# Kernel optimization log

Hardware: AMD Instinct MI355X
Metric: run time of the kernel (lower is better)

The kernel has to match this reference:

```python
import math
import jax, jax.numpy as jnp
import numpy as np

DIM = 2048
HEAD_DIM = 64
N_HEADS = DIM // HEAD_DIM
BATCH = 4
SEQ = 1025  # 32*32 axial positions + 1 zero position
EPS = 1e-6


def make_theta(head_dim=HEAD_DIM, h=32, w=32):
    # freqs: geometric from pi to 10*pi, head_dim//4 of them
    n_freqs = head_dim // 4
    freqs = jnp.exp(jnp.linspace(math.log(math.pi), math.log(10 * math.pi), n_freqs))
    hp = jnp.linspace(-1.0, 1.0, h + 1)
    wp = jnp.linspace(-1.0, 1.0, w + 1)
    hp = (hp[:-1] + hp[1:]) / 2
    wp = (wp[:-1] + wp[1:]) / 2
    pos = jnp.stack(jnp.meshgrid(hp, wp, indexing='ij'), axis=-1).reshape(h * w, 2)
    pos = jnp.concatenate([jnp.zeros((1, 2)), pos], axis=0)  # [1025, 2]
    theta_h = pos[:, 0:1] * freqs  # [S, n_freqs]
    theta_w = pos[:, 1:2] * freqs
    return jnp.concatenate([theta_h, theta_w], axis=-1)  # [S, head_dim//2]


def rms_norm(x, scale, eps=EPS):
    mean_sq = jnp.mean(jnp.square(x.astype(jnp.float32)), axis=-1, keepdims=True)
    s = scale.astype(jnp.float32) * jax.lax.rsqrt(mean_sq + eps)
    return (x * s.astype(x.dtype)).astype(x.dtype)


def apply_rotary(x, theta):
    # x: [B, H, S, D], theta: [S, d] with 2*d <= D
    d = theta.shape[-1]
    x1, x2, x3 = x[..., :d], x[..., d:2 * d], x[..., 2 * d:]
    cos, sin = jnp.cos(theta), jnp.sin(theta)  # broadcast over B, H
    y1 = x1 * cos - x2 * sin
    y2 = x2 * cos + x1 * sin
    return jnp.concatenate([y1, y2, x3], axis=-1)


def setup_inputs() -> dict:
    key = jax.random.key(0)
    k1, k2, k3 = jax.random.split(key, 3)
    x = jax.random.normal(k1, (BATCH, SEQ, DIM), dtype=jnp.float32)
    scale = jnp.ones((DIM,), dtype=jnp.float32)
    w_qkv = jax.random.normal(k2, (3 * DIM, DIM), dtype=jnp.float32) * 0.02
    w_out = jax.random.normal(k3, (DIM, DIM), dtype=jnp.float32) * 0.02
    return {"x": x, "scale": scale, "w_qkv": w_qkv, "w_out": w_out}


def reference(x, scale, w_qkv, w_out):
    B, S, _ = x.shape
    skip = x
    h = rms_norm(x, scale)
    qkv = h @ w_qkv.T  # [B, S, 3*DIM]
    qkv = qkv.reshape(B, S, 3, N_HEADS, HEAD_DIM)
    qkv = jnp.transpose(qkv, (0, 3, 2, 1, 4))  # [B, H, 3, S, D]
    q, k, v = qkv[:, :, 0], qkv[:, :, 1], qkv[:, :, 2]
    theta = make_theta()[:S]
    q = apply_rotary(q, theta)
    k = apply_rotary(k, theta)
    scores = jnp.einsum('bhqd,bhkd->bhqk', q, k) / math.sqrt(HEAD_DIM)
    causal = jnp.tril(jnp.ones((S, S), dtype=bool))
    scores = jnp.where(causal, scores, jnp.finfo(scores.dtype).min)
    attn = jax.nn.softmax(scores, axis=-1)
    o = jnp.einsum('bhqk,bhkd->bhqd', attn, v)  # [B, H, S, D]
    o = jnp.transpose(o, (0, 2, 1, 3)).reshape(B, S, DIM)
    return o @ w_out.T + skip
```

## Files before the change

kernel.cpp:

```cpp
#include <hip/hip_runtime.h>
#include <hip/hip_bf16.h>
#include <cstdint>

#define SEQ   1025
#define SPAD  1088
#define DIM   2048
#define NQKV  6144
#define MROWS 4100
#define MPAD  4352
#define NH    32

typedef __attribute__((ext_vector_type(8))) short bf16x8;
typedef __attribute__((ext_vector_type(4))) short bf16x4;
typedef __attribute__((ext_vector_type(4))) float f32x4;

#define MFMA16x16(A,B,C) __builtin_amdgcn_mfma_f32_16x16x32_bf16(A,B,C,0,0,0)

static __device__ __forceinline__ float bf2f(short s) {
    union { unsigned int u; float f; } v;
    v.u = ((unsigned int)(unsigned short)s) << 16;
    return v.f;
}
static __device__ __forceinline__ short f2bf(float f) {
    union { float f; unsigned int u; } v; v.f = f;
    unsigned int r = v.u + 0x7fffu + ((v.u >> 16) & 1u);
    return (short)(r >> 16);
}

typedef __attribute__((address_space(1))) unsigned int u32g;
typedef __attribute__((address_space(3))) unsigned int u32l;
static __device__ __forceinline__ void gld_lds16(void* lds, const void* g) {
    __builtin_amdgcn_global_load_lds((const u32g*)(uintptr_t)g,
                                     (u32l*)(uintptr_t)lds, 16, 0, 0);
}

#define SBX() __builtin_amdgcn_sched_barrier(0)
#define PRIO(x) __builtin_amdgcn_s_setprio(x)
#define VMCNT(n) asm volatile("s_waitcnt vmcnt(" #n ")" ::: "memory")
#define LGKM(n)  asm volatile("s_waitcnt lgkmcnt(" #n ")" ::: "memory")

__global__ __launch_bounds__(256) void trig_k(float* __restrict__ cosT, float* __restrict__ sinT) {
    int i = blockIdx.x * 256 + threadIdx.x;
    if (i >= SEQ * 16) return;
    int s = i >> 4, f = i & 15;
    float ph = 0.f, pw = 0.f;
    if (s > 0) {
        int p = s - 1;
        ph = -1.f + ((p >> 5) + 0.5f) * 0.0625f;
        pw = -1.f + ((p & 31) + 0.5f) * 0.0625f;
    }
    double fr = 3.141592653589793 * exp((double)f * 0.15350567286626973);
    float th = (float)(ph * fr), tw = (float)(pw * fr);
    cosT[s*32 + f]      = cosf(th);
    sinT[s*32 + f]      = sinf(th);
    cosT[s*32 + 16 + f] = cosf(tw);
    sinT[s*32 + 16 + f] = sinf(tw);
}

__global__ __launch_bounds__(256) void rmsnorm_k(const float* __restrict__ x,
                                                 const float* __restrict__ sc,
                                                 short* __restrict__ h) {
    int row = blockIdx.x, t = threadIdx.x;
    short* hr = h + (size_t)row * DIM;
    if (row >= MROWS) {
        bf16x8 z = {};
        *(bf16x8*)(hr + t*8) = z;
        return;
    }
    const float4* xr = (const float4*)(x + (size_t)row * DIM);
    float4 a = xr[2*t], b = xr[2*t+1];
    float ss = a.x*a.x + a.y*a.y + a.z*a.z + a.w*a.w
             + b.x*b.x + b.y*b.y + b.z*b.z + b.w*b.w;
    #pragma unroll
    for (int off = 32; off; off >>= 1) ss += __shfl_xor(ss, off, 64);
    __shared__ float red[4];
    if ((t & 63) == 0) red[t >> 6] = ss;
    __syncthreads();
    float ms = (red[0]+red[1]+red[2]+red[3]) * (1.0f/2048.0f);
    float inv = rsqrtf(ms + 1e-6f);
    const float4* sr = (const float4*)sc;
    float4 s0 = sr[2*t], s1 = sr[2*t+1];
    bf16x8 o;
    o[0]=f2bf(a.x*(s0.x*inv)); o[1]=f2bf(a.y*(s0.y*inv));
    o[2]=f2bf(a.z*(s0.z*inv)); o[3]=f2bf(a.w*(s0.w*inv));
    o[4]=f2bf(b.x*(s1.x*inv)); o[5]=f2bf(b.y*(s1.y*inv));
    o[6]=f2bf(b.z*(s1.z*inv)); o[7]=f2bf(b.w*(s1.w*inv));
    *(bf16x8*)(hr + t*8) = o;
}

__global__ __launch_bounds__(256) void conv2_k(const float* __restrict__ a, short* __restrict__ oa, int n4a,
                                               const float* __restrict__ b, short* __restrict__ ob, int n4b) {
    int i = blockIdx.x * 256 + threadIdx.x;
    const float* src; short* dst; int j;
    if (i < n4a) { src = a; dst = oa; j = i; }
    else { j = i - n4a; if (j >= n4b) return; src = b; dst = ob; }
    float4 v = ((const float4*)src)[j];
    bf16x4 r = { f2bf(v.x), f2bf(v.y), f2bf(v.z), f2bf(v.w) };
    *(bf16x4*)(dst + (size_t)j*4) = r;
}

template<int EPI>
__global__ __launch_bounds__(512, 2) void gemm8p(const short* __restrict__ A,
                                                 const short* __restrict__ B,
                                                 void* __restrict__ C,
                                                 const float* __restrict__ skip,
                                                 int N, int K, int nbm) {
    extern __shared__ char smem[];
    const int nwg = gridDim.x;
    const int cpx = nwg >> 3;
    const int bid = blockIdx.x;
    const int sid = (bid & 7) * cpx + (bid >> 3);
    const int bm = sid % nbm;
    const int bn = sid / nbm;

    const int t = threadIdx.x, w = t >> 6, l = t & 63;
    const int lr = l & 15, lg = l >> 4;
    const int wr = w >> 2, wc = w & 3;

    const short* Ab = A + (size_t)bm * 256 * K;
    const short* Bb = B + (size_t)bn * 256 * K;

    const int srow = t >> 3;
    const int scol = (((t & 7) ^ (srow & 7)) << 3);

    const int cs0 = (lg * 16) ^ ((lr & 7) << 4);
    const int cs1 = (64 + lg * 16) ^ ((lr & 7) << 4);
    const int aBase = wr * 16384 + lr * 128;
    const int bBase = 32768 + (wc >> 1) * 16384 + ((wc & 1) * 64 + lr) * 128;

    f32x4 acc[8][4] = {};
    bf16x8 rA[4][2], rB01[2][2], rB23[2][2];

#define STAGE_A(kt, half, bb) do {                                            \
    const int k0_ = (kt) * 64;                                                \
    gld_lds16(smem + (bb)*65536 + (half)*16384 + (w<<10),                     \
              Ab + (size_t)((half)*128 + srow) * K + k0_ + scol);             \
    gld_lds16(smem + (bb)*65536 + (half)*16384 + 8192 + (w<<10),              \
              Ab + (size_t)((half)*128 + 64 + srow) * K + k0_ + scol);        \
} while (0)

#define STAGE_B(kt, half, bb) do {                                            \
    const int k0_ = (kt) * 64;                                                \
    gld_lds16(smem + (bb)*65536 + 32768 + (half)*16384 + (w<<10),             \
              Bb + (size_t)((half)*128 + srow) * K + k0_ + scol);             \
    gld_lds16(smem + (bb)*65536 + 32768 + (half)*16384 + 8192 + (w<<10),      \
              Bb + (size_t)((half)*128 + 64 + srow) * K + k0_ + scol);        \
} while (0)

#define READ_A(bb, h) do {                                                    \
    const char* p_ = smem + (bb)*65536 + aBase + (h)*8192;                    \
    _Pragma("unroll")                                                         \
    for (int am = 0; am < 4; ++am) {                                          \
        rA[am][0] = *(const bf16x8*)(p_ + am*2048 + cs0);                     \
        rA[am][1] = *(const bf16x8*)(p_ + am*2048 + cs1);                     \
    }                                                                         \
} while (0)

#define READ_B(bb, np, arr) do {                                              \
    const char* p_ = smem + (bb)*65536 + bBase + (np)*4096;                   \
    _Pragma("unroll")                                                         \
    for (int nn = 0; nn < 2; ++nn) {                                          \
        arr[nn][0] = *(const bf16x8*)(p_ + nn*2048 + cs0);                    \
        arr[nn][1] = *(const bf16x8*)(p_ + nn*2048 + cs1);                    \
    }                                                                         \
} while (0)

#define MF_Q(h, np, arr) do {                                                 \
    _Pragma("unroll")                                                         \
    for (int am = 0; am < 4; ++am)                                            \
    _Pragma("unroll")                                                         \
    for (int nn = 0; nn < 2; ++nn) {                                          \
        acc[(h)*4+am][(np)*2+nn] =                                            \
            MFMA16x16(rA[am][0], arr[nn][0], acc[(h)*4+am][(np)*2+nn]);       \
        acc[(h)*4+am][(np)*2+nn] =                                            \
            MFMA16x16(rA[am][1], arr[nn][1], acc[(h)*4+am][(np)*2+nn]);       \
    }                                                                         \
} while (0)

#define BOPEN()  do { SBX(); __builtin_amdgcn_s_barrier(); LGKM(0); SBX(); } while (0)
#define BOPEN_NL() do { SBX(); __builtin_amdgcn_s_barrier(); SBX(); } while (0)
#define BCLOSE() do { SBX(); __builtin_amdgcn_s_barrier(); SBX(); } while (0)

    STAGE_B(0, 0, 0); STAGE_B(0, 1, 0);
    STAGE_A(0, 0, 0); STAGE_A(0, 1, 0);
    STAGE_B(1, 0, 1); STAGE_B(1, 1, 1);
    VMCNT(4); SBX();
    __builtin_amdgcn_s_barrier(); SBX();

    const int NT2 = K / 128;
    for (int it = 0; it < NT2; ++it) {
        const bool more = (it < NT2 - 1);
        READ_A(0, 0); READ_B(0, 0, rB01);
        STAGE_A(2*it + 1, 0, 1);
        LGKM(8);
        BOPEN(); PRIO(1); MF_Q(0, 0, rB01); PRIO(0); BCLOSE();
        READ_B(0, 1, rB23);
        STAGE_A(2*it + 1, 1, 1);
        BOPEN(); PRIO(1); MF_Q(0, 1, rB23); PRIO(0); BCLOSE();
        READ_A(0, 1);
        if (more) STAGE_B(2*it + 2, 0, 0);
        BOPEN(); PRIO(1); MF_Q(1, 1, rB23); PRIO(0); BCLOSE();
        if (more) STAGE_B(2*it + 2, 1, 0);
        BOPEN_NL(); PRIO(1); MF_Q(1, 0, rB01); PRIO(0); SBX();
        if (more) { VMCNT(4); } else { VMCNT(0); }
        BCLOSE();
        READ_A(1, 0); READ_B(1, 0, rB01);
        if (more) STAGE_A(2*it + 2, 0, 0);
        LGKM(8);
        BOPEN(); PRIO(1); MF_Q(0, 0, rB01); PRIO(0); BCLOSE();
        READ_B(1, 1, rB23);
        if (more) STAGE_A(2*it + 2, 1, 0);
        BOPEN(); PRIO(1); MF_Q(0, 1, rB23); PRIO(0); BCLOSE();
        READ_A(1, 1);
        if (more) STAGE_B(2*it + 3, 0, 1);
        BOPEN(); PRIO(1); MF_Q(1, 1, rB23); PRIO(0); BCLOSE();
        if (more) STAGE_B(2*it + 3, 1, 1);
        BOPEN_NL(); PRIO(1); MF_Q(1, 0, rB01); PRIO(0); SBX();
        if (more) { VMCNT(4); }
        BCLOSE();
    }

    #pragma unroll
    for (int m = 0; m < 8; ++m) {
        const int row0 = bm*256 + wr*128 + m*16 + lg*4;
        #pragma unroll
        for (int n = 0; n < 4; ++n) {
            const int col = bn*256 + wc*64 + n*16 + lr;
            #pragma unroll
            for (int r = 0; r < 4; ++r) {
                const int row = row0 + r;
                if constexpr (EPI == 0) {
                    ((short*)C)[(size_t)row * N + col] = f2bf(acc[m][n][r]);
                } else {
                    if (row < MROWS)
                        ((float*)C)[(size_t)row * N + col] =
                            acc[m][n][r] + skip[(size_t)row * N + col];
                }
            }
        }
    }
#undef STAGE_A
#undef STAGE_B
#undef READ_A
#undef READ_B
#undef MF_Q
#undef BOPEN
#undef BOPEN_NL
#undef BCLOSE
}

__global__ __launch_bounds__(256) void rearrange_k(const short* __restrict__ qkv,
        const float* __restrict__ cosT, const float* __restrict__ sinT,
        short* __restrict__ kr, short* __restrict__ vt) {
    int bid = blockIdx.x;
    int bh = bid / 17, st = bid % 17;
    int b = bh >> 5, hh = bh & 31;
    int s0 = st * 64;
    int t = threadIdx.x;
    __shared__ short vs[64][68];
    #pragma unroll
    for (int i = 0; i < 8; ++i) {
        int task = t + i*256;
        int sl = task >> 5, p = task & 31;
        int s = s0 + sl;
        float y1 = 0.f, y2 = 0.f;
        if (s < SEQ) {
            const short* src = qkv + (size_t)(b*SEQ + s)*NQKV + DIM + hh*64;
            float x1 = bf2f(src[p]), x2 = bf2f(src[32+p]);
            float c = cosT[s*32+p], sn = sinT[s*32+p];
            y1 = x1*c - x2*sn;
            y2 = x2*c + x1*sn;
        }
        short* dst = kr + ((size_t)bh*SPAD + s)*64;
        dst[p]    = f2bf(y1);
        dst[32+p] = f2bf(y2);
    }
    #pragma unroll
    for (int i = 0; i < 16; ++i) {
        int task = t + i*256;
        int sl = task >> 6, d = task & 63;
        int s = s0 + sl;
        short v = 0;
        if (s < SEQ) v = qkv[(size_t)(b*SEQ + s)*NQKV + 2*DIM + hh*64 + d];
        vs[sl][d] = v;
    }
    __syncthreads();
    #pragma unroll
    for (int i = 0; i < 16; ++i) {
        int task = t + i*256;
        int d = task >> 6, sl = task & 63;
        vt[((size_t)bh*64 + d)*SPAD + s0 + sl] = vs[sl][d];
    }
}

__global__ __launch_bounds__(256) void attn_k(const short* __restrict__ qkv,
        const short* __restrict__ kr, const short* __restrict__ vt,
        const float* __restrict__ cosT, const float* __restrict__ sinT,
        short* __restrict__ ob) {
    const int nwg = gridDim.x;
    const int cpx = nwg >> 3;
    const int bid = blockIdx.x;
    const int sid = (bid & 7) * cpx + (bid >> 3);
    const int bh = sid / 17;
    const int qt = sid % 17;
    const int q0 = qt * 64;
    const int b = bh >> 5, hh = bh & 31;
    const int t = threadIdx.x, w = t >> 6, l = t & 63;
    const int lr = l & 15, lg = l >> 4;

    __shared__ short Ks[2][64*64];
    __shared__ short Vts[2][64*64];

    const int qrow = q0 + w*16 + lr;
    const int qc = qrow < SEQ ? qrow : SEQ-1;
    const short* qsrc = qkv + (size_t)(b*SEQ + qc)*NQKV + hh*64;
    bf16x8 xlo = *(const bf16x8*)(qsrc + lg*8);
    bf16x8 xhi = *(const bf16x8*)(qsrc + 32 + lg*8);
    const float4* cp = (const float4*)(cosT + qc*32 + lg*8);
    const float4* sp = (const float4*)(sinT + qc*32 + lg*8);
    float cc[8], sn[8];
    { float4 u = cp[0], v2 = cp[1];
      cc[0]=u.x; cc[1]=u.y; cc[2]=u.z; cc[3]=u.w;
      cc[4]=v2.x; cc[5]=v2.y; cc[6]=v2.z; cc[7]=v2.w; }
    { float4 u = sp[0], v2 = sp[1];
      sn[0]=u.x; sn[1]=u.y; sn[2]=u.z; sn[3]=u.w;
      sn[4]=v2.x; sn[5]=v2.y; sn[6]=v2.z; sn[7]=v2.w; }
    bf16x8 qf0, qf1;
    #pragma unroll
    for (int j = 0; j < 8; ++j) {
        float x1 = bf2f(xlo[j]), x2 = bf2f(xhi[j]);
        qf0[j] = f2bf(x1*cc[j] - x2*sn[j]);
        qf1[j] = f2bf(x2*cc[j] + x1*sn[j]);
    }

    f32x4 oacc[4] = {};
    float mrun = -1e30f, lrun = 0.f;
    const int ntile = qt + 1;
    const float SC = 0.125f * 1.4426950408889634f;

    const char* kbase = (const char*)(kr + (size_t)bh * SPAD * 64);
    const char* vbase = (const char*)(vt + (size_t)bh * 64 * SPAD);
    const int srow8 = l >> 3;
    const int sslotB = ((l & 7) ^ srow8) << 4;
    const int swz = (lr & 7) << 4;

#define STAGE_KV(kt, c) do {                                                   \
    const int kv0_ = (kt) * 64;                                                \
    gld_lds16((char*)Ks[c] + w*2048,                                           \
              kbase + (size_t)(kv0_ + w*16 + srow8)*128 + sslotB);             \
    gld_lds16((char*)Ks[c] + w*2048 + 1024,                                    \
              kbase + (size_t)(kv0_ + w*16 + 8 + srow8)*128 + sslotB);         \
    gld_lds16((char*)Vts[c] + w*2048,                                          \
              vbase + (size_t)(w*16 + srow8)*(SPAD*2) + (size_t)kv0_*2 + sslotB); \
    gld_lds16((char*)Vts[c] + w*2048 + 1024,                                   \
              vbase + (size_t)(w*16 + 8 + srow8)*(SPAD*2) + (size_t)kv0_*2 + sslotB); \
} while (0)

    STAGE_KV(0, 0);

    for (int kt = 0; kt < ntile; ++kt) {
        const int kv0 = kt * 64;
        const int cur = kt & 1;
        if (kt + 1 < ntile) { STAGE_KV(kt + 1, cur ^ 1); SBX(); VMCNT(4); }
        else { SBX(); VMCNT(0); }
        SBX(); __builtin_amdgcn_s_barrier(); SBX();

        f32x4 st[4];
        #pragma unroll
        for (int f = 0; f < 4; ++f) {
            const char* kp = (const char*)Ks[cur] + (f*16 + lr)*128;
            bf16x8 a0 = *(const bf16x8*)(kp + ((lg*16) ^ swz));
            bf16x8 a1 = *(const bf16x8*)(kp + ((64 + lg*16) ^ swz));
            f32x4 z = {};
            z = MFMA16x16(a0, qf0, z);
            st[f] = MFMA16x16(a1, qf1, z);
        }

        float pv[16];
        float tmax = -1e30f;
        #pragma unroll
        for (int f = 0; f < 4; ++f)
        #pragma unroll
        for (int r = 0; r < 4; ++r) {
            int kv = kv0 + f*16 + lg*4 + r;
            float v = st[f][r] * SC;
            v = (kv <= qrow && kv < SEQ) ? v : -1e30f;
            pv[f*4+r] = v; tmax = fmaxf(tmax, v);
        }
        tmax = fmaxf(tmax, __shfl_xor(tmax, 16, 64));
        tmax = fmaxf(tmax, __shfl_xor(tmax, 32, 64));
        float mnew = fmaxf(mrun, tmax);
        float alpha = exp2f(mrun - mnew);
        float psum = 0.f;
        bf16x8 pf0, pf1;
        #pragma unroll
        for (int j = 0; j < 4; ++j) {
            float p0 = exp2f(pv[0*4+j] - mnew);
            float p1 = exp2f(pv[1*4+j] - mnew);
            float p2 = exp2f(pv[2*4+j] - mnew);
            float p3 = exp2f(pv[3*4+j] - mnew);
            psum += (p0 + p1) + (p2 + p3);
            pf0[j] = f2bf(p0); pf0[4+j] = f2bf(p1);
            pf1[j] = f2bf(p2); pf1[4+j] = f2bf(p3);
        }
        psum += __shfl_xor(psum, 16, 64);
        psum += __shfl_xor(psum, 32, 64);
        lrun = lrun * alpha + psum;
        mrun = mnew;
        #pragma unroll
        for (int df = 0; df < 4; ++df) {
            oacc[df][0] *= alpha; oacc[df][1] *= alpha;
            oacc[df][2] *= alpha; oacc[df][3] *= alpha;
        }
        #pragma unroll
        for (int df = 0; df < 4; ++df) {
            const char* vp = (const char*)Vts[cur] + (df*16 + lr)*128;
            bf16x4 v0 = *(const bf16x4*)(vp + ((lg*8) ^ swz));
            bf16x4 v1 = *(const bf16x4*)(vp + ((32 + lg*8) ^ swz));
            bf16x4 v2 = *(const bf16x4*)(vp + ((64 + lg*8) ^ swz));
            bf16x4 v3 = *(const bf16x4*)(vp + ((96 + lg*8) ^ swz));
            bf16x8 vf0, vf1;
            vf0[0]=v0[0]; vf0[1]=v0[1]; vf0[2]=v0[2]; vf0[3]=v0[3];
            vf0[4]=v1[0]; vf0[5]=v1[1]; vf0[6]=v1[2]; vf0[7]=v1[3];
            vf1[0]=v2[0]; vf1[1]=v2[1]; vf1[2]=v2[2]; vf1[3]=v2[3];
            vf1[4]=v3[0]; vf1[5]=v3[1]; vf1[6]=v3[2]; vf1[7]=v3[3];
            oacc[df] = MFMA16x16(vf0, pf0, oacc[df]);
            oacc[df] = MFMA16x16(vf1, pf1, oacc[df]);
        }
        SBX(); __builtin_amdgcn_s_barrier(); SBX();
    }
#undef STAGE_KV

    if (qrow < SEQ) {
        float inv = 1.0f / lrun;
        short* orow = ob + (size_t)(b*SEQ + qrow)*DIM + hh*64;
        #pragma unroll
        for (int df = 0; df < 4; ++df) {
            bf16x4 ov = { f2bf(oacc[df][0]*inv), f2bf(oacc[df][1]*inv),
                          f2bf(oacc[df][2]*inv), f2bf(oacc[df][3]*inv) };
            *(bf16x4*)(orow + df*16 + lg*4) = ov;
        }
    }
}

extern "C" void kernel_launch(void* const* d_in, const int* in_sizes, int n_in,
                              void* d_out, int out_size, void* d_ws, size_t ws_size,
                              hipStream_t stream) {
    const float* x     = (const float*)d_in[0];
    const float* scale = (const float*)d_in[1];
    const float* w_qkv = (const float*)d_in[2];
    const float* w_out = (const float*)d_in[3];
    float* out = (float*)d_out;

    char* ws = (char*)d_ws;
    size_t off = 0;
    auto alloc = [&](size_t bytes) -> char* {
        char* p = ws + off;
        off += (bytes + 255) & ~(size_t)255;
        return p;
    };
    float* cosT  = (float*)alloc((size_t)SEQ*32*4);
    float* sinT  = (float*)alloc((size_t)SEQ*32*4);
    short* h_b   = (short*)alloc((size_t)MPAD*DIM*2);
    short* wq_b  = (short*)alloc((size_t)NQKV*DIM*2);
    short* wo_b  = (short*)alloc((size_t)DIM*DIM*2);
    short* qkv_b = (short*)alloc((size_t)MPAD*NQKV*2);
    short* k_r   = (short*)alloc((size_t)128*SPAD*64*2);
    short* vt    = (short*)alloc((size_t)128*SPAD*64*2);
    short* o_b   = h_b;

    hipFuncSetAttribute((const void*)gemm8p<0>,
                        hipFuncAttributeMaxDynamicSharedMemorySize, 131072);
    hipFuncSetAttribute((const void*)gemm8p<1>,
                        hipFuncAttributeMaxDynamicSharedMemorySize, 131072);

    trig_k<<<65, 256, 0, stream>>>(cosT, sinT);
    rmsnorm_k<<<MPAD, 256, 0, stream>>>(x, scale, h_b);
    conv2_k<<<(NQKV*DIM/4 + DIM*DIM/4 + 255)/256, 256, 0, stream>>>(
        w_qkv, wq_b, NQKV*DIM/4, w_out, wo_b, DIM*DIM/4);
    gemm8p<0><<<(MPAD/256)*(NQKV/256), 512, 131072, stream>>>(h_b, wq_b, qkv_b, nullptr, NQKV, DIM, MPAD/256);
    rearrange_k<<<128*17, 256, 0, stream>>>(qkv_b, cosT, sinT, k_r, vt);
    attn_k<<<17*128, 256, 0, stream>>>(qkv_b, k_r, vt, cosT, sinT, o_b);
    gemm8p<1><<<(MPAD/256)*(DIM/256), 512, 131072, stream>>>(o_b, wo_b, out, x, DIM, DIM, MPAD/256);
}
```

Baseline: 440.1 us.

## Load K/V fragments directly from global into registers, dropping LDS staging

The attention kernel no longer stages K and V^T tiles through double-buffered shared memory with barriers. Each wave now loads its MFMA fragments straight from global memory into registers, software-pipelining the K fragments across two register sets and loading V fragments at the start of each tile. This removes LDS traffic and the two block barriers per tile, but each of the four waves now fetches the full K/V tile itself (4x global/L2 traffic) and register pressure grows.

Result: slower. 621.9 us (+41.3%).

```diff
diff --git a/kernel.cpp b/kernel.cpp
--- a/kernel.cpp
+++ b/kernel.cpp
@@ -308,9 +308,6 @@
     const int t = threadIdx.x, w = t >> 6, l = t & 63;
     const int lr = l & 15, lg = l >> 4;
 
-    __shared__ short Ks[2][64*64];
-    __shared__ short Vts[2][64*64];
-
     const int qrow = q0 + w*16 + lr;
     const int qc = qrow < SEQ ? qrow : SEQ-1;
     const short* qsrc = qkv + (size_t)(b*SEQ + qc)*NQKV + hh*64;
@@ -338,98 +335,96 @@
     const int ntile = qt + 1;
     const float SC = 0.125f * 1.4426950408889634f;
 
-    const char* kbase = (const char*)(kr + (size_t)bh * SPAD * 64);
-    const char* vbase = (const char*)(vt + (size_t)bh * 64 * SPAD);
-    const int srow8 = l >> 3;
-    const int sslotB = ((l & 7) ^ srow8) << 4;
-    const int swz = (lr & 7) << 4;
-
-#define STAGE_KV(kt, c) do {                                                   \
-    const int kv0_ = (kt) * 64;                                                \
-    gld_lds16((char*)Ks[c] + w*2048,                                           \
-              kbase + (size_t)(kv0_ + w*16 + srow8)*128 + sslotB);             \
-    gld_lds16((char*)Ks[c] + w*2048 + 1024,                                    \
-              kbase + (size_t)(kv0_ + w*16 + 8 + srow8)*128 + sslotB);         \
-    gld_lds16((char*)Vts[c] + w*2048,                                          \
-              vbase + (size_t)(w*16 + srow8)*(SPAD*2) + (size_t)kv0_*2 + sslotB); \
-    gld_lds16((char*)Vts[c] + w*2048 + 1024,                                   \
-              vbase + (size_t)(w*16 + 8 + srow8)*(SPAD*2) + (size_t)kv0_*2 + sslotB); \
-} while (0)
-
-    STAGE_KV(0, 0);
-
-    for (int kt = 0; kt < ntile; ++kt) {
-        const int kv0 = kt * 64;
-        const int cur = kt & 1;
-        if (kt + 1 < ntile) { STAGE_KV(kt + 1, cur ^ 1); SBX(); VMCNT(4); }
-        else { SBX(); VMCNT(0); }
-        SBX(); __builtin_amdgcn_s_barrier(); SBX();
-
-        f32x4 st[4];
-        #pragma unroll
-        for (int f = 0; f < 4; ++f) {
-            const char* kp = (const char*)Ks[cur] + (f*16 + lr)*128;
-            bf16x8 a0 = *(const bf16x8*)(kp + ((lg*16) ^ swz));
-            bf16x8 a1 = *(const bf16x8*)(kp + ((64 + lg*16) ^ swz));
-            f32x4 z = {};
-            z = MFMA16x16(a0, qf0, z);
-            st[f] = MFMA16x16(a1, qf1, z);
-        }
-
-        float pv[16];
-        float tmax = -1e30f;
-        #pragma unroll
-        for (int f = 0; f < 4; ++f)
-        #pragma unroll
-        for (int r = 0; r < 4; ++r) {
-            int kv = kv0 + f*16 + lg*4 + r;
-            float v = st[f][r] * SC;
-            v = (kv <= qrow && kv < SEQ) ? v : -1e30f;
-            pv[f*4+r] = v; tmax = fmaxf(tmax, v);
-        }
-        tmax = fmaxf(tmax, __shfl_xor(tmax, 16, 64));
-        tmax = fmaxf(tmax, __shfl_xor(tmax, 32, 64));
-        float mnew = fmaxf(mrun, tmax);
-        float alpha = exp2f(mrun - mnew);
-        float psum = 0.f;
-        bf16x8 pf0, pf1;
-        #pragma unroll
-        for (int j = 0; j < 4; ++j) {
-            float p0 = exp2f(pv[0*4+j] - mnew);
-            float p1 = exp2f(pv[1*4+j] - mnew);
-            float p2 = exp2f(pv[2*4+j] - mnew);
-            float p3 = exp2f(pv[3*4+j] - mnew);
-            psum += (p0 + p1) + (p2 + p3);
-            pf0[j] = f2bf(p0); pf0[4+j] = f2bf(p1);
-            pf1[j] = f2bf(p2); pf1[4+j] = f2bf(p3);
-        }
-        psum += __shfl_xor(psum, 16, 64);
-        psum += __shfl_xor(psum, 32, 64);
-        lrun = lrun * alpha + psum;
-        mrun = mnew;
-        #pragma unroll
-        for (int df = 0; df < 4; ++df) {
-            oacc[df][0] *= alpha; oacc[df][1] *= alpha;
-            oacc[df][2] *= alpha; oacc[df][3] *= alpha;
-        }
-        #pragma unroll
-        for (int df = 0; df < 4; ++df) {
-            const char* vp = (const char*)Vts[cur] + (df*16 + lr)*128;
-            bf16x4 v0 = *(const bf16x4*)(vp + ((lg*8) ^ swz));
-            bf16x4 v1 = *(const bf16x4*)(vp + ((32 + lg*8) ^ swz));
-            bf16x4 v2 = *(const bf16x4*)(vp + ((64 + lg*8) ^ swz));
-            bf16x4 v3 = *(const bf16x4*)(vp + ((96 + lg*8) ^ swz));
-            bf16x8 vf0, vf1;
-            vf0[0]=v0[0]; vf0[1]=v0[1]; vf0[2]=v0[2]; vf0[3]=v0[3];
-            vf0[4]=v1[0]; vf0[5]=v1[1]; vf0[6]=v1[2]; vf0[7]=v1[3];
-            vf1[0]=v2[0]; vf1[1]=v2[1]; vf1[2]=v2[2]; vf1[3]=v2[3];
-            vf1[4]=v3[0]; vf1[5]=v3[1]; vf1[6]=v3[2]; vf1[7]=v3[3];
-            oacc[df] = MFMA16x16(vf0, pf0, oacc[df]);
-            oacc[df] = MFMA16x16(vf1, pf1, oacc[df]);
-        }
-        SBX(); __builtin_amdgcn_s_barrier(); SBX();
-    }
-#undef STAGE_KV
+    const char* kfp = (const char*)(kr + (size_t)bh * SPAD * 64) + (size_t)lr*128 + lg*16;
+    const char* vfp = (const char*)(vt + (size_t)bh * 64 * SPAD) + (size_t)lr*2176 + lg*8;
+
+#define LOADK(dst, kt_) do {                                                   \
+    const char* kp_ = kfp + (size_t)(kt_) * 8192;                              \
+    _Pragma("unroll")                                                          \
+    for (int f = 0; f < 4; ++f) {                                              \
+        dst[f*2]   = *(const bf16x8*)(kp_ + f*2048);                           \
+        dst[f*2+1] = *(const bf16x8*)(kp_ + f*2048 + 64);                      \
+    }                                                                          \
+} while (0)
+
+#define BODY(ka, kt_) do {                                                     \
+    const int kv0 = (kt_) * 64;                                                \
+                             \
+    bf16x4 vv[16];                                                             \
+    { const char* vp_ = vfp + (size_t)kv0 * 2;                                 \
+      _Pragma("unroll")                                                        \
+      for (int df = 0; df < 4; ++df)                                           \
+      _Pragma("unroll")                                                        \
+      for (int s2 = 0; s2 < 4; ++s2)                                           \
+          vv[df*4+s2] = *(const bf16x4*)(vp_ + (size_t)df*16*2176 + s2*32); }  \
+    f32x4 st[4];                                                               \
+    _Pragma("unroll")                                                          \
+    for (int f = 0; f < 4; ++f) {                                              \
+        f32x4 z = {};                                                          \
+        z = MFMA16x16(ka[f*2], qf0, z);                                        \
+        st[f] = MFMA16x16(ka[f*2+1], qf1, z);                                  \
+    }                                                                          \
+    float tmax = -1e30f;                                                       \
+    _Pragma("unroll")                                                          \
+    for (int f = 0; f < 4; ++f)                                                \
+    _Pragma("unroll")                                                          \
+    for (int r = 0; r < 4; ++r) {                                              \
+        int kv = kv0 + f*16 + lg*4 + r;                                        \
+        float v = st[f][r] * SC;                                               \
+        v = (kv <= qrow && kv < SEQ) ? v : -1e30f;                             \
+        st[f][r] = v; tmax = fmaxf(tmax, v);                                   \
+    }                                                                          \
+    tmax = fmaxf(tmax, __shfl_xor(tmax, 16, 64));                              \
+    tmax = fmaxf(tmax, __shfl_xor(tmax, 32, 64));                              \
+    float mnew = fmaxf(mrun, tmax);                                            \
+    float alpha = exp2f(mrun - mnew);                                          \
+    float psum = 0.f;                                                          \
+    bf16x8 pf0, pf1;                                                           \
+    _Pragma("unroll")                                                          \
+    for (int j = 0; j < 4; ++j) {                                              \
+        float p0 = exp2f(st[0][j] - mnew);                                     \
+        float p1 = exp2f(st[1][j] - mnew);                                     \
+        float p2 = exp2f(st[2][j] - mnew);                                     \
+        float p3 = exp2f(st[3][j] - mnew);                                     \
+        psum += (p0 + p1) + (p2 + p3);                                         \
+        pf0[j] = f2bf(p0); pf0[4+j] = f2bf(p1);                                \
+        pf1[j] = f2bf(p2); pf1[4+j] = f2bf(p3);                                \
+    }                                                                          \
+    psum += __shfl_xor(psum, 16, 64);                                          \
+    psum += __shfl_xor(psum, 32, 64);                                          \
+    lrun = lrun * alpha + psum;                                                \
+    mrun = mnew;                                                               \
+    _Pragma("unroll")                                                          \
+    for (int df = 0; df < 4; ++df) {                                           \
+        oacc[df][0] *= alpha; oacc[df][1] *= alpha;                            \
+        oacc[df][2] *= alpha; oacc[df][3] *= alpha;                            \
+    }                                                                          \
+    _Pragma("unroll")                                                          \
+    for (int df = 0; df < 4; ++df) {                                           \
+        bf16x8 vf0, vf1;                                                       \
+        bf16x4 a_ = vv[df*4+0], b_ = vv[df*4+1], c_ = vv[df*4+2], d_ = vv[df*4+3]; \
+        vf0[0]=a_[0]; vf0[1]=a_[1]; vf0[2]=a_[2]; vf0[3]=a_[3];                \
+        vf0[4]=b_[0]; vf0[5]=b_[1]; vf0[6]=b_[2]; vf0[7]=b_[3];                \
+        vf1[0]=c_[0]; vf1[1]=c_[1]; vf1[2]=c_[2]; vf1[3]=c_[3];                \
+        vf1[4]=d_[0]; vf1[5]=d_[1]; vf1[6]=d_[2]; vf1[7]=d_[3];                \
+        oacc[df] = MFMA16x16(vf0, pf0, oacc[df]);                              \
+        oacc[df] = MFMA16x16(vf1, pf1, oacc[df]);                              \
+    }                                                                          \
+} while (0)
+
+    bf16x8 kA[8], kB[8];
+    LOADK(kA, 0);
+    int kt = 0;
+    for (;;) {
+        if (kt + 1 < ntile) LOADK(kB, kt + 1);
+        BODY(kA, kt);
+        ++kt; if (kt >= ntile) break;
+        if (kt + 1 < ntile) LOADK(kA, kt + 1);
+        BODY(kB, kt);
+        ++kt; if (kt >= ntile) break;
+    }
+#undef LOADK
+#undef BODY
 
     if (qrow < SEQ) {
         float inv = 1.0f / lrun;
```

## Double attention query tile per workgroup and fuse prologue kernels into one launch

Applied to the files above, without the earlier changes.

Attention workgroups now process 128 query rows, with each wave computing two 16-row groups against the same staged K/V tiles. This halves K/V LDS staging per query, and tiles are scheduled longest-first. The rmsnorm, weight conversion and trig table kernels are merged into a single launch to cut launch overhead. The wider tile raises register pressure and does some extra masked work on the causal diagonal.

After: 450.5 us. 2.3% more time.

```diff
diff --git a/kernel.cpp b/kernel.cpp
--- a/kernel.cpp
+++ b/kernel.cpp
@@ -39,8 +39,57 @@
 #define VMCNT(n) asm volatile("s_waitcnt vmcnt(" #n ")" ::: "memory")
 #define LGKM(n)  asm volatile("s_waitcnt lgkmcnt(" #n ")" ::: "memory")
 
-__global__ __launch_bounds__(256) void trig_k(float* __restrict__ cosT, float* __restrict__ sinT) {
-    int i = blockIdx.x * 256 + threadIdx.x;
+__global__ __launch_bounds__(256) void prep_k(const float* __restrict__ x,
+        const float* __restrict__ sc, short* __restrict__ h,
+        const float* __restrict__ wq, short* __restrict__ wqb,
+        const float* __restrict__ wo, short* __restrict__ wob,
+        float* __restrict__ cosT, float* __restrict__ sinT) {
+    __shared__ float red[4];
+    int blk = blockIdx.x, t = threadIdx.x;
+    if (blk < MPAD) {
+        int row = blk;
+        short* hr = h + (size_t)row * DIM;
+        if (row >= MROWS) {
+            bf16x8 z = {};
+            *(bf16x8*)(hr + t*8) = z;
+            return;
+        }
+        const float4* xr = (const float4*)(x + (size_t)row * DIM);
+        float4 a = xr[2*t], b2 = xr[2*t+1];
+        float ss = a.x*a.x + a.y*a.y + a.z*a.z + a.w*a.w
+                 + b2.x*b2.x + b2.y*b2.y + b2.z*b2.z + b2.w*b2.w;
+        #pragma unroll
+        for (int off = 32; off; off >>= 1) ss += __shfl_xor(ss, off, 64);
+        if ((t & 63) == 0) red[t >> 6] = ss;
+        __syncthreads();
+        float ms = (red[0]+red[1]+red[2]+red[3]) * (1.0f/2048.0f);
+        float inv = rsqrtf(ms + 1e-6f);
+        const float4* sr = (const float4*)sc;
+        float4 s0 = sr[2*t], s1 = sr[2*t+1];
+        bf16x8 o;
+        o[0]=f2bf(a.x*(s0.x*inv));  o[1]=f2bf(a.y*(s0.y*inv));
+        o[2]=f2bf(a.z*(s0.z*inv));  o[3]=f2bf(a.w*(s0.w*inv));
+        o[4]=f2bf(b2.x*(s1.x*inv)); o[5]=f2bf(b2.y*(s1.y*inv));
+        o[6]=f2bf(b2.z*(s1.z*inv)); o[7]=f2bf(b2.w*(s1.w*inv));
+        *(bf16x8*)(hr + t*8) = o;
+        return;
+    }
+    blk -= MPAD;
+    constexpr int N4A = NQKV*DIM/4;
+    constexpr int N4B = DIM*DIM/4;
+    constexpr int NCB = (N4A + N4B + 255)/256;
+    if (blk < NCB) {
+        int i = blk*256 + t;
+        const float* src; short* dst; int j;
+        if (i < N4A) { src = wq; dst = wqb; j = i; }
+        else { j = i - N4A; if (j >= N4B) return; src = wo; dst = wob; }
+        float4 v = ((const float4*)src)[j];
+        bf16x4 r = { f2bf(v.x), f2bf(v.y), f2bf(v.z), f2bf(v.w) };
+        *(bf16x4*)(dst + (size_t)j*4) = r;
+        return;
+    }
+    blk -= NCB;
+    int i = blk*256 + t;
     if (i >= SEQ * 16) return;
     int s = i >> 4, f = i & 15;
     float ph = 0.f, pw = 0.f;
@@ -55,48 +104,6 @@
     sinT[s*32 + f]      = sinf(th);
     cosT[s*32 + 16 + f] = cosf(tw);
     sinT[s*32 + 16 + f] = sinf(tw);
-}
-
-__global__ __launch_bounds__(256) void rmsnorm_k(const float* __restrict__ x,
-                                                 const float* __restrict__ sc,
-                                                 short* __restrict__ h) {
-    int row = blockIdx.x, t = threadIdx.x;
-    short* hr = h + (size_t)row * DIM;
-    if (row >= MROWS) {
-        bf16x8 z = {};
-        *(bf16x8*)(hr + t*8) = z;
-        return;
-    }
-    const float4* xr = (const float4*)(x + (size_t)row * DIM);
-    float4 a = xr[2*t], b = xr[2*t+1];
-    float ss = a.x*a.x + a.y*a.y + a.z*a.z + a.w*a.w
-             + b.x*b.x + b.y*b.y + b.z*b.z + b.w*b.w;
-    #pragma unroll
-    for (int off = 32; off; off >>= 1) ss += __shfl_xor(ss, off, 64);
-    __shared__ float red[4];
-    if ((t & 63) == 0) red[t >> 6] = ss;
-    __syncthreads();
-    float ms = (red[0]+red[1]+red[2]+red[3]) * (1.0f/2048.0f);
-    float inv = rsqrtf(ms + 1e-6f);
-    const float4* sr = (const float4*)sc;
-    float4 s0 = sr[2*t], s1 = sr[2*t+1];
-    bf16x8 o;
-    o[0]=f2bf(a.x*(s0.x*inv)); o[1]=f2bf(a.y*(s0.y*inv));
-    o[2]=f2bf(a.z*(s0.z*inv)); o[3]=f2bf(a.w*(s0.w*inv));
-    o[4]=f2bf(b.x*(s1.x*inv)); o[5]=f2bf(b.y*(s1.y*inv));
-    o[6]=f2bf(b.z*(s1.z*inv)); o[7]=f2bf(b.w*(s1.w*inv));
-    *(bf16x8*)(hr + t*8) = o;
-}
-
-__global__ __launch_bounds__(256) void conv2_k(const float* __restrict__ a, short* __restrict__ oa, int n4a,
-                                               const float* __restrict__ b, short* __restrict__ ob, int n4b) {
-    int i = blockIdx.x * 256 + threadIdx.x;
-    const float* src; short* dst; int j;
-    if (i < n4a) { src = a; dst = oa; j = i; }
-    else { j = i - n4a; if (j >= n4b) return; src = b; dst = ob; }
-    float4 v = ((const float4*)src)[j];
-    bf16x4 r = { f2bf(v.x), f2bf(v.y), f2bf(v.z), f2bf(v.w) };
-    *(bf16x4*)(dst + (size_t)j*4) = r;
 }
 
 template<int EPI>
@@ -301,9 +308,9 @@
     const int cpx = nwg >> 3;
     const int bid = blockIdx.x;
     const int sid = (bid & 7) * cpx + (bid >> 3);
-    const int bh = sid / 17;
-    const int qt = sid % 17;
-    const int q0 = qt * 64;
+    const int bh = sid / 9;
+    const int qt = 8 - (sid % 9);
+    const int q0 = qt * 128;
     const int b = bh >> 5, hh = bh & 31;
     const int t = threadIdx.x, w = t >> 6, l = t & 63;
     const int lr = l & 15, lg = l >> 4;
@@ -311,31 +318,35 @@
     __shared__ short Ks[2][64*64];
     __shared__ short Vts[2][64*64];
 
-    const int qrow = q0 + w*16 + lr;
-    const int qc = qrow < SEQ ? qrow : SEQ-1;
-    const short* qsrc = qkv + (size_t)(b*SEQ + qc)*NQKV + hh*64;
-    bf16x8 xlo = *(const bf16x8*)(qsrc + lg*8);
-    bf16x8 xhi = *(const bf16x8*)(qsrc + 32 + lg*8);
-    const float4* cp = (const float4*)(cosT + qc*32 + lg*8);
-    const float4* sp = (const float4*)(sinT + qc*32 + lg*8);
-    float cc[8], sn[8];
-    { float4 u = cp[0], v2 = cp[1];
-      cc[0]=u.x; cc[1]=u.y; cc[2]=u.z; cc[3]=u.w;
-      cc[4]=v2.x; cc[5]=v2.y; cc[6]=v2.z; cc[7]=v2.w; }
-    { float4 u = sp[0], v2 = sp[1];
-      sn[0]=u.x; sn[1]=u.y; sn[2]=u.z; sn[3]=u.w;
-      sn[4]=v2.x; sn[5]=v2.y; sn[6]=v2.z; sn[7]=v2.w; }
-    bf16x8 qf0, qf1;
-    #pragma unroll
-    for (int j = 0; j < 8; ++j) {
-        float x1 = bf2f(xlo[j]), x2 = bf2f(xhi[j]);
-        qf0[j] = f2bf(x1*cc[j] - x2*sn[j]);
-        qf1[j] = f2bf(x2*cc[j] + x1*sn[j]);
-    }
-
-    f32x4 oacc[4] = {};
-    float mrun = -1e30f, lrun = 0.f;
-    const int ntile = qt + 1;
+    const int qrowA = q0 + w*32 + lr;
+    const int qrowB = qrowA + 16;
+
+    bf16x8 qf0A, qf1A, qf0B, qf1B;
+    auto loadq = [&](int qrow, bf16x8& f0, bf16x8& f1) {
+        int qc = qrow < SEQ ? qrow : SEQ-1;
+        const short* qsrc = qkv + (size_t)(b*SEQ + qc)*NQKV + hh*64;
+        bf16x8 xlo = *(const bf16x8*)(qsrc + lg*8);
+        bf16x8 xhi = *(const bf16x8*)(qsrc + 32 + lg*8);
+        float4 c0 = ((const float4*)(cosT + qc*32 + lg*8))[0];
+        float4 c1 = ((const float4*)(cosT + qc*32 + lg*8))[1];
+        float4 s0 = ((const float4*)(sinT + qc*32 + lg*8))[0];
+        float4 s1 = ((const float4*)(sinT + qc*32 + lg*8))[1];
+        float cc[8] = {c0.x,c0.y,c0.z,c0.w,c1.x,c1.y,c1.z,c1.w};
+        float sn[8] = {s0.x,s0.y,s0.z,s0.w,s1.x,s1.y,s1.z,s1.w};
+        #pragma unroll
+        for (int j = 0; j < 8; ++j) {
+            float x1 = bf2f(xlo[j]), x2 = bf2f(xhi[j]);
+            f0[j] = f2bf(x1*cc[j] - x2*sn[j]);
+            f1[j] = f2bf(x2*cc[j] + x1*sn[j]);
+        }
+    };
+    loadq(qrowA, qf0A, qf1A);
+    loadq(qrowB, qf0B, qf1B);
+
+    f32x4 oaccA[4] = {}, oaccB[4] = {};
+    float mrunA = -1e30f, lrunA = 0.f;
+    float mrunB = -1e30f, lrunB = 0.f;
+    const int ntile = min(2*qt + 2, 17);
     const float SC = 0.125f * 1.4426950408889634f;
 
     const char* kbase = (const char*)(kr + (size_t)bh * SPAD * 64);
@@ -344,8 +355,8 @@
     const int sslotB = ((l & 7) ^ srow8) << 4;
     const int swz = (lr & 7) << 4;
 
-#define STAGE_KV(kt, c) do {                                                   \
-    const int kv0_ = (kt) * 64;                                                \
+#define STAGE_KV(kt_, c) do {                                                  \
+    const int kv0_ = (kt_) * 64;                                               \
     gld_lds16((char*)Ks[c] + w*2048,                                           \
               kbase + (size_t)(kv0_ + w*16 + srow8)*128 + sslotB);             \
     gld_lds16((char*)Ks[c] + w*2048 + 1024,                                    \
@@ -356,6 +367,38 @@
               vbase + (size_t)(w*16 + 8 + srow8)*(SPAD*2) + (size_t)kv0_*2 + sslotB); \
 } while (0)
 
+#define SOFTMAX(st, qrow, pf0, pf1, mrun, lrun, alpha) do {                    \
+    float tmax = -1e30f;                                                       \
+    _Pragma("unroll")                                                          \
+    for (int f = 0; f < 4; ++f)                                                \
+    _Pragma("unroll")                                                          \
+    for (int r = 0; r < 4; ++r) {                                              \
+        int kv = kv0 + f*16 + lg*4 + r;                                        \
+        float v = st[f][r] * SC;                                               \
+        v = (kv <= (qrow) && kv < SEQ) ? v : -1e30f;                           \
+        st[f][r] = v; tmax = fmaxf(tmax, v);                                   \
+    }                                                                          \
+    tmax = fmaxf(tmax, __shfl_xor(tmax, 16, 64));                              \
+    tmax = fmaxf(tmax, __shfl_xor(tmax, 32, 64));                              \
+    float mnew = fmaxf(mrun, tmax);                                            \
+    alpha = exp2f(mrun - mnew);                                                \
+    float psum = 0.f;                                                          \
+    _Pragma("unroll")                                                          \
+    for (int j = 0; j < 4; ++j) {                                              \
+        float p0 = exp2f(st[0][j] - mnew);                                     \
+        float p1 = exp2f(st[1][j] - mnew);                                     \
+        float p2 = exp2f(st[2][j] - mnew);                                     \
+        float p3 = exp2f(st[3][j] - mnew);                                     \
+        psum += (p0 + p1) + (p2 + p3);                                         \
+        pf0[j] = f2bf(p0); pf0[4+j] = f2bf(p1);                                \
+        pf1[j] = f2bf(p2); pf1[4+j] = f2bf(p3);                                \
+    }                                                                          \
+    psum += __shfl_xor(psum, 16, 64);                                          \
+    psum += __shfl_xor(psum, 32, 64);                                          \
+    lrun = lrun * alpha + psum;                                                \
+    mrun = mnew;                                                               \
+} while (0)
+
     STAGE_KV(0, 0);
 
     for (int kt = 0; kt < ntile; ++kt) {
@@ -365,53 +408,33 @@
         else { SBX(); VMCNT(0); }
         SBX(); __builtin_amdgcn_s_barrier(); SBX();
 
-        f32x4 st[4];
+        f32x4 stA[4], stB[4];
         #pragma unroll
         for (int f = 0; f < 4; ++f) {
             const char* kp = (const char*)Ks[cur] + (f*16 + lr)*128;
             bf16x8 a0 = *(const bf16x8*)(kp + ((lg*16) ^ swz));
             bf16x8 a1 = *(const bf16x8*)(kp + ((64 + lg*16) ^ swz));
-            f32x4 z = {};
-            z = MFMA16x16(a0, qf0, z);
-            st[f] = MFMA16x16(a1, qf1, z);
-        }
-
-        float pv[16];
-        float tmax = -1e30f;
-        #pragma unroll
-        for (int f = 0; f < 4; ++f)
-        #pragma unroll
-        for (int r = 0; r < 4; ++r) {
-            int kv = kv0 + f*16 + lg*4 + r;
-            float v = st[f][r] * SC;
-            v = (kv <= qrow && kv < SEQ) ? v : -1e30f;
-            pv[f*4+r] = v; tmax = fmaxf(tmax, v);
-        }
-        tmax = fmaxf(tmax, __shfl_xor(tmax, 16, 64));
-        tmax = fmaxf(tmax, __shfl_xor(tmax, 32, 64));
-        float mnew = fmaxf(mrun, tmax);
-        float alpha = exp2f(mrun - mnew);
-        float psum = 0.f;
-        bf16x8 pf0, pf1;
-        #pragma unroll
-        for (int j = 0; j < 4; ++j) {
-            float p0 = exp2f(pv[0*4+j] - mnew);
-            float p1 = exp2f(pv[1*4+j] - mnew);
-            float p2 = exp2f(pv[2*4+j] - mnew);
-            float p3 = exp2f(pv[3*4+j] - mnew);
-            psum += (p0 + p1) + (p2 + p3);
-            pf0[j] = f2bf(p0); pf0[4+j] = f2bf(p1);
-            pf1[j] = f2bf(p2); pf1[4+j] = f2bf(p3);
-        }
-        psum += __shfl_xor(psum, 16, 64);
-        psum += __shfl_xor(psum, 32, 64);
-        lrun = lrun * alpha + psum;
-        mrun = mnew;
+            f32x4 zA = {};
+            zA = MFMA16x16(a0, qf0A, zA);
+            stA[f] = MFMA16x16(a1, qf1A, zA);
+            f32x4 zB = {};
+            zB = MFMA16x16(a0, qf0B, zB);
+            stB[f] = MFMA16x16(a1, qf1B, zB);
+        }
+
+        bf16x8 pfA0, pfA1, pfB0, pfB1;
+        float alphaA, alphaB;
+        SOFTMAX(stA, qrowA, pfA0, pfA1, mrunA, lrunA, alphaA);
+        SOFTMAX(stB, qrowB, pfB0, pfB1, mrunB, lrunB, alphaB);
+
         #pragma unroll
         for (int df = 0; df < 4; ++df) {
-            oacc[df][0] *= alpha; oacc[df][1] *= alpha;
-            oacc[df][2] *= alpha; oacc[df][3] *= alpha;
-        }
+            oaccA[df][0] *= alphaA; oaccA[df][1] *= alphaA;
+            oaccA[df][2] *= alphaA; oaccA[df][3] *= alphaA;
+            oaccB[df][0] *= alphaB; oaccB[df][1] *= alphaB;
+            oaccB[df][2] *= alphaB; oaccB[df][3] *= alphaB;
+        }
+
         #pragma unroll
         for (int df = 0; df < 4; ++df) {
             const char* vp = (const char*)Vts[cur] + (df*16 + lr)*128;
@@ -424,23 +447,30 @@
             vf0[4]=v1[0]; vf0[5]=v1[1]; vf0[6]=v1[2]; vf0[7]=v1[3];
             vf1[0]=v2[0]; vf1[1]=v2[1]; vf1[2]=v2[2]; vf1[3]=v2[3];
             vf1[4]=v3[0]; vf1[5]=v3[1]; vf1[6]=v3[2]; vf1[7]=v3[3];
-            oacc[df] = MFMA16x16(vf0, pf0, oacc[df]);
-            oacc[df] = MFMA16x16(vf1, pf1, oacc[df]);
+            oaccA[df] = MFMA16x16(vf0, pfA0, oaccA[df]);
+            oaccA[df] = MFMA16x16(vf1, pfA1, oaccA[df]);
+            oaccB[df] = MFMA16x16(vf0, pfB0, oaccB[df]);
+            oaccB[df] = MFMA16x16(vf1, pfB1, oaccB[df]);
         }
         SBX(); __builtin_amdgcn_s_barrier(); SBX();
     }
 #undef STAGE_KV
-
-    if (qrow < SEQ) {
-        float inv = 1.0f / lrun;
-        short* orow = ob + (size_t)(b*SEQ + qrow)*DIM + hh*64;
-        #pragma unroll
-        for (int df = 0; df < 4; ++df) {
-            bf16x4 ov = { f2bf(oacc[df][0]*inv), f2bf(oacc[df][1]*inv),
-                          f2bf(oacc[df][2]*inv), f2bf(oacc[df][3]*inv) };
-            *(bf16x4*)(orow + df*16 + lg*4) = ov;
-        }
-    }
+#undef SOFTMAX
+
+    auto writeo = [&](int qrow, const f32x4* oacc, float lrun) {
+        if (qrow < SEQ) {
+            float inv = 1.0f / lrun;
+            short* orow = ob + (size_t)(b*SEQ + qrow)*DIM + hh*64;
+            #pragma unroll
+            for (int df = 0; df < 4; ++df) {
+                bf16x4 ov = { f2bf(oacc[df][0]*inv), f2bf(oacc[df][1]*inv),
+                              f2bf(oacc[df][2]*inv), f2bf(oacc[df][3]*inv) };
+                *(bf16x4*)(orow + df*16 + lg*4) = ov;
+            }
+        }
+    };
+    writeo(qrowA, oaccA, lrunA);
+    writeo(qrowB, oaccB, lrunB);
 }
 
 extern "C" void kernel_launch(void* const* d_in, const int* in_sizes, int n_in,
@@ -474,12 +504,11 @@
     hipFuncSetAttribute((const void*)gemm8p<1>,
                         hipFuncAttributeMaxDynamicSharedMemorySize, 131072);
 
-    trig_k<<<65, 256, 0, stream>>>(cosT, sinT);
-    rmsnorm_k<<<MPAD, 256, 0, stream>>>(x, scale, h_b);
-    conv2_k<<<(NQKV*DIM/4 + DIM*DIM/4 + 255)/256, 256, 0, stream>>>(
-        w_qkv, wq_b, NQKV*DIM/4, w_out, wo_b, DIM*DIM/4);
+    constexpr int NCB = (NQKV*DIM/4 + DIM*DIM/4 + 255)/256;
+    prep_k<<<MPAD + NCB + 65, 256, 0, stream>>>(x, scale, h_b,
+                                                w_qkv, wq_b, w_out, wo_b, cosT, sinT);
     gemm8p<0><<<(MPAD/256)*(NQKV/256), 512, 131072, stream>>>(h_b, wq_b, qkv_b, nullptr, NQKV, DIM, MPAD/256);
     rearrange_k<<<128*17, 256, 0, stream>>>(qkv_b, cosT, sinT, k_r, vt);
-    attn_k<<<17*128, 256, 0, stream>>>(qkv_b, k_r, vt, cosT, sinT, o_b);
+    attn_k<<<128*9, 256, 0, stream>>>(qkv_b, k_r, vt, cosT, sinT, o_b);
     gemm8p<1><<<(MPAD/256)*(DIM/256), 512, 131072, stream>>>(o_b, wo_b, out, x, DIM, DIM, MPAD/256);
 }
```
